# Optimization experiments

Measured on AMD Instinct MI355X. Metric: run time of the kernel, lower is better.

## Reference

```python
import jax, jax.numpy as jnp
import numpy as np

# Config: b=2, n=1024, dim=512, heads=8, dim_head=64, L=8 slices/head, temperature=0.1

def setup_inputs() -> dict:
    key = jax.random.key(0)
    ks = jax.random.split(key, 5)
    b, n, dim = 2, 1024, 512
    heads, dim_head, L = 8, 64, 8
    inner = heads * dim_head
    x = jax.random.normal(ks[0], (b, n, dim), jnp.float32)
    W_qkv = jax.random.normal(ks[1], (dim, 3 * inner), jnp.float32) * 0.02
    theta = jax.random.normal(ks[2], (heads, L, dim_head), jnp.float32)
    W_out = jax.random.normal(ks[3], (inner, dim), jnp.float32) * 0.02
    b_out = jnp.zeros((dim,), jnp.float32)
    return {"x": x, "W_qkv": W_qkv, "theta": theta, "W_out": W_out, "b_out": b_out}


def reference(x, W_qkv, theta, W_out, b_out):
    b, n, dim = x.shape
    heads, L, dim_head = theta.shape
    scale = dim_head ** -0.5
    temperature = 0.1
    # QKV projection (no bias) and head split: b n (h d) -> b h n d
    qkv = x @ W_qkv
    q, k, v = jnp.split(qkv, 3, axis=-1)
    sh = lambda t: t.reshape(b, n, heads, dim_head).transpose(0, 2, 1, 3)
    q = sh(q) * scale
    k = sh(k) * scale
    v = sh(v)
    # Esp: learnable unit slice directions per head, 1D projections
    th = theta / jnp.linalg.norm(theta, axis=-1, keepdims=True)  # [h, L, d]
    qp = jnp.einsum('bhnd,hld->bhln', q, th)  # [b,h,L,n]
    kp = jnp.einsum('bhnd,hld->bhln', k, th)
    # per-slice soft 1D transport plan (rows sum to 1), averaged over slices,
    # scaled to total-mass-1 plan (rows sum 1/n)
    d2 = (qp[..., :, None] - kp[..., None, :]) ** 2  # [b,h,L,n,n]
    plans = jax.nn.softmax(-d2 / temperature, axis=-1)
    P = plans.mean(axis=2) / n  # [b,h,n,n], rows sum to 1/n
    # SA: attn = attn * attn.shape[-1] -> row-stochastic
    attn = P * n
    out = jnp.einsum('bhnm,bhmd->bhnd', attn, v)
    out = out.transpose(0, 2, 1, 3).reshape(b, n, heads * dim_head)
    out = out @ W_out + b_out  # to_out Linear (dropout=0 in eval)
    return out, attn
```

## Files before the change

kernel.cpp:

```cpp
#include <hip/hip_runtime.h>
#include <hip/hip_bf16.h>

#define CEXP (-14.4269504088896340736f)

typedef __attribute__((ext_vector_type(8))) short bfrag8;
typedef __attribute__((ext_vector_type(4))) float fvec4;
typedef __attribute__((ext_vector_type(8))) unsigned short ushort8;
typedef __attribute__((ext_vector_type(4))) unsigned short ushort4v;

__device__ inline unsigned short f2bf(float f) {
    unsigned u = __builtin_bit_cast(unsigned, f);
    u += 0x7fffu + ((u >> 16) & 1u);
    return (unsigned short)(u >> 16);
}
__device__ inline float bf2f(unsigned short h) {
    unsigned u = ((unsigned)h) << 16;
    return __builtin_bit_cast(float, u);
}

template <int CTRL, int RMASK>
__device__ __forceinline__ float dpp_add(float v) {
    int m = __builtin_amdgcn_update_dpp(0, __builtin_bit_cast(int, v), CTRL, RMASK, 0xf, true);
    return v + __builtin_bit_cast(float, m);
}
__device__ __forceinline__ float wave_sum64(float v) {
    v = dpp_add<0xB1,  0xf>(v);
    v = dpp_add<0x4E,  0xf>(v);
    v = dpp_add<0x141, 0xf>(v);
    v = dpp_add<0x140, 0xf>(v);
    v = dpp_add<0x142, 0xa>(v);
    v = dpp_add<0x143, 0xc>(v);
    return __builtin_bit_cast(float, __builtin_amdgcn_readlane(__builtin_bit_cast(int, v), 63));
}

__global__ __launch_bounds__(256) void k_wproj(const float* __restrict__ Wqkv,
                                               const float* __restrict__ theta,
                                               const float* __restrict__ Wout,
                                               unsigned short* __restrict__ WThi,
                                               unsigned short* __restrict__ WTlo,
                                               unsigned short* __restrict__ WoThi,
                                               unsigned short* __restrict__ WoTlo) {
    __shared__ float th_s[64 * 65];
    __shared__ float ts2[64 * 65];
    __shared__ float tq[4][64];
    __shared__ float tk[4][64];
    __shared__ float wvs[4][512];
    int tid = threadIdx.x;
    int hl = tid & 63, cl = tid >> 6;
    #pragma unroll
    for (int i = 0; i < 16; ++i) {
        int r = cl * 16 + i;
        th_s[r * 65 + hl] = theta[r * 64 + hl];
    }
    __syncthreads();
    const float* ts = th_s + hl * 65;
    float ss = 0.f;
    #pragma unroll 8
    for (int d = 0; d < 64; ++d) ss = fmaf(ts[d], ts[d], ss);
    float inv = rsqrtf(ss);
    int c0b = blockIdx.x * 4;
    int c = c0b + cl;
    int h = hl >> 3;
    const float* wq = Wqkv + c * 1536 + h * 64;
    const float* wk = wq + 512;
    float aq = 0.f, ak = 0.f;
    #pragma unroll 4
    for (int d = 0; d < 64; ++d) {
        float tv = ts[d];
        aq = fmaf(wq[d], tv, aq);
        ak = fmaf(wk[d], tv, ak);
    }
    tq[cl][hl] = aq * inv;
    tk[cl][hl] = ak * inv;

    {
        const float4* src = (const float4*)(Wqkv + 1024);
        #pragma unroll
        for (int j = 0; j < 2; ++j) {
            int idx = j * 256 + tid;
            int rloc = idx >> 7, o4 = idx & 127;
            float4 v = src[(c0b + rloc) * 384 + o4];
            *(float4*)(&wvs[rloc][o4 * 4]) = v;
        }
    }
    __syncthreads();

    {
        int n = tid & 63, g = tid >> 6;
        const float (*tp)[64] = (g < 2) ? tq : tk;
        float vsrc[4];
        #pragma unroll
        for (int j = 0; j < 4; ++j) vsrc[j] = tp[j][n];
        ushort4v st;
        if ((g & 1) == 0) {
            #pragma unroll
            for (int j = 0; j < 4; ++j) st[j] = f2bf(vsrc[j]);
        } else {
            #pragma unroll
            for (int j = 0; j < 4; ++j) {
                unsigned short hi = f2bf(vsrc[j]);
                st[j] = f2bf(vsrc[j] - bf2f(hi));
            }
        }
        unsigned short* base = ((g & 1) == 0) ? WThi : WTlo;
        int nrow = (g < 2) ? n : (64 + n);
        *(ushort4v*)(base + (size_t)nrow * 512 + c0b) = st;
    }
    #pragma unroll
    for (int j2 = 0; j2 < 2; ++j2) {
        int n = j2 * 256 + tid;
        ushort4v h4, l4;
        #pragma unroll
        for (int k = 0; k < 4; ++k) {
            float v = wvs[k][n];
            unsigned short hi = f2bf(v);
            h4[k] = hi;
            l4[k] = f2bf(v - bf2f(hi));
        }
        *(ushort4v*)(WThi + (size_t)(128 + n) * 512 + c0b) = h4;
        *(ushort4v*)(WTlo + (size_t)(128 + n) * 512 + c0b) = l4;
    }

    if (blockIdx.x < 64) {
        int r0 = (blockIdx.x >> 3) * 64;
        int c0 = (blockIdx.x & 7) * 64;
        int cc = tid & 63, rr = tid >> 6;
        #pragma unroll
        for (int k = 0; k < 16; ++k) {
            int r = rr + 4 * k;
            ts2[r * 65 + cc] = Wout[(r0 + r) * 512 + c0 + cc];
        }
        __syncthreads();
        int kk = tid & 63, nn = tid >> 6;
        #pragma unroll
        for (int i = 0; i < 16; ++i) {
            int n = nn + 4 * i;
            float v = ts2[kk * 65 + n];
            unsigned short hi = f2bf(v);
            WoThi[(size_t)(c0 + n) * 512 + r0 + kk] = hi;
            WoTlo[(size_t)(c0 + n) * 512 + r0 + kk] = f2bf(v - bf2f(hi));
        }
    }
}

__global__ __launch_bounds__(256) void k_proj(const float* __restrict__ x,
                                              const unsigned short* __restrict__ WThi,
                                              const unsigned short* __restrict__ WTlo,
                                              float* __restrict__ qp,
                                              float* __restrict__ kp,
                                              unsigned short* __restrict__ vThi,
                                              unsigned short* __restrict__ vTlo) {
    __shared__ unsigned short ps[32 * 512];
    int blk = blockIdx.x;
    int cs = blk % 5;
    int rg = blk / 5;
    int tid = threadIdx.x;
    int w = tid >> 6, lane = tid & 63;

    const float4* xg = (const float4*)(x + (size_t)rg * 16 * 512);
    #pragma unroll
    for (int rep = 0; rep < 8; ++rep) {
        int idx = rep * 256 + tid;
        int row = idx >> 7, c4 = idx & 127;
        float4 v = xg[idx];
        int swz = (row & 7) << 3;
        int cbase = c4 * 4;
        ushort4v h4, l4;
        float vv[4] = {v.x, v.y, v.z, v.w};
        #pragma unroll
        for (int jj = 0; jj < 4; ++jj) {
            unsigned short hi = f2bf(vv[jj]);
            h4[jj] = hi;
            l4[jj] = f2bf(vv[jj] - bf2f(hi));
        }
        *(ushort4v*)(ps + row * 512 + (cbase ^ swz))        = h4;
        *(ushort4v*)(ps + (row + 16) * 512 + (cbase ^ swz)) = l4;
    }
    __syncthreads();

    int ar  = lane & 15;
    int asw = (ar & 7) << 3;
    int ak  = (lane >> 4) * 8;
    const unsigned short* aph = ps + ar * 512;
    const unsigned short* apl = ps + (ar + 16) * 512;
    int colb = cs * 128 + w * 32;
    size_t b0 = (size_t)(colb + ar) * 512 + ak;
    size_t b1 = b0 + 16 * 512;
    fvec4 acc0 = {0.f, 0.f, 0.f, 0.f};
    fvec4 acc1 = {0.f, 0.f, 0.f, 0.f};
    #pragma unroll 4
    for (int s = 0; s < 16; ++s) {
        int ko = s * 32 + ak;
        bfrag8 ahi = *(const bfrag8*)(aph + (ko ^ asw));
        bfrag8 alo = *(const bfrag8*)(apl + (ko ^ asw));
        bfrag8 bh0 = *(const bfrag8*)(WThi + b0 + s * 32);
        bfrag8 bl0 = *(const bfrag8*)(WTlo + b0 + s * 32);
        bfrag8 bh1 = *(const bfrag8*)(WThi + b1 + s * 32);
        bfrag8 bl1 = *(const bfrag8*)(WTlo + b1 + s * 32);
        acc0 = __builtin_amdgcn_mfma_f32_16x16x32_bf16(ahi, bh0, acc0, 0, 0, 0);
        acc0 = __builtin_amdgcn_mfma_f32_16x16x32_bf16(ahi, bl0, acc0, 0, 0, 0);
        acc0 = __builtin_amdgcn_mfma_f32_16x16x32_bf16(alo, bh0, acc0, 0, 0, 0);
        acc1 = __builtin_amdgcn_mfma_f32_16x16x32_bf16(ahi, bh1, acc1, 0, 0, 0);
        acc1 = __builtin_amdgcn_mfma_f32_16x16x32_bf16(ahi, bl1, acc1, 0, 0, 0);
        acc1 = __builtin_amdgcn_mfma_f32_16x16x32_bf16(alo, bh1, acc1, 0, 0, 0);
    }

    int rowb = rg * 16 + (lane >> 4) * 4;
    int b = rowb >> 10, n = rowb & 1023;
    fvec4 accs[2] = {acc0, acc1};
    #pragma unroll
    for (int t = 0; t < 2; ++t) {
        int col = colb + t * 16 + ar;
        fvec4 a = accs[t];
        if (col < 128) {
            int hl = col & 63;
            float* dstp = (col < 64) ? qp : kp;
            fvec4 st;
            st[0] = a[0] * 0.125f; st[1] = a[1] * 0.125f;
            st[2] = a[2] * 0.125f; st[3] = a[3] * 0.125f;
            *(fvec4*)(dstp + ((size_t)((b * 8 + (hl >> 3)) * 8 + (hl & 7))) * 1024 + n) = st;
        } else {
            int vcol = col - 128;
            int h = vcol >> 6, d = vcol & 63;
            ushort4v h4, l4;
            #pragma unroll
            for (int q = 0; q < 4; ++q) {
                unsigned short hi = f2bf(a[q]);
                h4[q] = hi;
                l4[q] = f2bf(a[q] - bf2f(hi));
            }
            size_t off = (size_t)(b * 8 + h) * 65536 + (size_t)d * 1024 + n;
            *(ushort4v*)(vThi + off) = h4;
            *(ushort4v*)(vTlo + off) = l4;
        }
    }
}

__global__ __launch_bounds__(512) void k_attn_pv(const float* __restrict__ qp,
                                                 const float* __restrict__ kp,
                                                 const unsigned short* __restrict__ vThi,
                                                 const unsigned short* __restrict__ vTlo,
                                                 float* __restrict__ attn,
                                                 unsigned short* __restrict__ ohhi,
                                                 unsigned short* __restrict__ ohlo) {
    __shared__ float s_buf[8 * 1024];
    __shared__ float sc[4 * 64 * 4];
    int bx = blockIdx.x;
    int idx = bx >> 3;
    int bh = (bx & 7) * 2 + (idx >> 7);
    int rowbase = (idx & 127) * 8;
    int tid = threadIdx.x;
    int w = tid >> 6, lane = tid & 63;

    const float4* kp4 = (const float4*)(kp + bh * 8192);
    float4* kps4 = (float4*)s_buf;
    #pragma unroll
    for (int k = 0; k < 4; ++k) kps4[k * 512 + tid] = kp4[k * 512 + tid];

    int r = rowbase + w;
    float qv[8];
    #pragma unroll
    for (int l = 0; l < 8; ++l) qv[l] = qp[bh * 8192 + l * 1024 + r];
    __syncthreads();

    const fvec4 CE4 = {CEXP, CEXP, CEXP, CEXP};
    fvec4 acc4[4];
    #pragma unroll
    for (int mm = 0; mm < 4; ++mm) acc4[mm] = (fvec4){0.f, 0.f, 0.f, 0.f};

    for (int l = 0; l < 8; ++l) {
        fvec4 kv4[4], e4[4];
        #pragma unroll
        for (int mm = 0; mm < 4; ++mm)
            kv4[mm] = *(const fvec4*)(s_buf + l * 1024 + mm * 256 + lane * 4);
        float sqs = -2.f * CEXP * qv[l];
        fvec4 sq4 = {sqs, sqs, sqs, sqs};
        fvec4 sum4 = {0.f, 0.f, 0.f, 0.f};
        #pragma unroll
        for (int mm = 0; mm < 4; ++mm) {
            fvec4 k2 = (kv4[mm] * kv4[mm]) * CE4;
            fvec4 t  = sq4 * kv4[mm] + k2;
            fvec4 e;
            e[0] = __builtin_amdgcn_exp2f(t[0]);
            e[1] = __builtin_amdgcn_exp2f(t[1]);
            e[2] = __builtin_amdgcn_exp2f(t[2]);
            e[3] = __builtin_amdgcn_exp2f(t[3]);
            e4[mm] = e;
            sum4 += e;
        }
        float s = (sum4[0] + sum4[1]) + (sum4[2] + sum4[3]);
        float inv = 0.125f * __builtin_amdgcn_rcpf(wave_sum64(s));
        fvec4 inv4 = {inv, inv, inv, inv};
        #pragma unroll
        for (int mm = 0; mm < 4; ++mm) acc4[mm] = e4[mm] * inv4 + acc4[mm];
    }

    __syncthreads();

    unsigned short* ps = (unsigned short*)s_buf;
    int swz = w << 3;
    #pragma unroll
    for (int mm = 0; mm < 4; ++mm) {
        ushort4v h4, l4;
        #pragma unroll
        for (int jj = 0; jj < 4; ++jj) {
            float v = acc4[mm][jj];
            unsigned short hi = f2bf(v);
            h4[jj] = hi;
            l4[jj] = f2bf(v - bf2f(hi));
        }
        int j0 = mm * 256 + lane * 4;
        *(ushort4v*)(ps + w * 1024 + (j0 ^ swz))       = h4;
        *(ushort4v*)(ps + (w + 8) * 1024 + (j0 ^ swz)) = l4;
    }
    __syncthreads();

    float* aR = attn + ((size_t)(bh * 1024 + r)) * 1024;
    #pragma unroll
    for (int mm = 0; mm < 4; ++mm)
        __builtin_nontemporal_store(acc4[mm], (fvec4*)(aR + mm * 256 + lane * 4));

    int n0 = (w & 3) * 16;
    int kh = w >> 2;
    int ar  = lane & 15;
    int asw = (ar & 7) << 3;
    int ak  = (lane >> 4) * 8;
    const unsigned short* ap = ps + ar * 1024;
    size_t boff = (size_t)bh * 65536 + (size_t)(n0 + ar) * 1024 + ak;
    const unsigned short* bh_p = vThi + boff;
    const unsigned short* bl_p = vTlo + boff;
    fvec4 c2 = {0.f, 0.f, 0.f, 0.f};
    #pragma unroll 4
    for (int s = kh * 16; s < kh * 16 + 16; ++s) {
        bfrag8 a  = *(const bfrag8*)(ap + ((s * 32 + ak) ^ asw));
        bfrag8 vh = *(const bfrag8*)(bh_p + s * 32);
        bfrag8 vl = *(const bfrag8*)(bl_p + s * 32);
        c2 = __builtin_amdgcn_mfma_f32_16x16x32_bf16(a, vh, c2, 0, 0, 0);
        c2 = __builtin_amdgcn_mfma_f32_16x16x32_bf16(a, vl, c2, 0, 0, 0);
    }
    if (w >= 4) {
        #pragma unroll
        for (int q = 0; q < 4; ++q) sc[(w - 4) * 256 + lane * 4 + q] = c2[q];
    }
    __syncthreads();
    if (w < 4) {
        int b = bh >> 3, h = bh & 7;
        #pragma unroll
        for (int q = 0; q < 4; ++q) {
            float t = c2[q] + sc[w * 256 + lane * 4 + q];
            t += __shfl_xor(t, 32);
            if (lane < 32) {
                int row = rowbase + (lane >> 4) * 4 + q;
                size_t o = (size_t)(b * 1024 + row) * 512 + h * 64 + n0 + ar;
                unsigned short hi = f2bf(t);
                ohhi[o] = hi;
                ohlo[o] = f2bf(t - bf2f(hi));
            }
        }
    }
}

__global__ __launch_bounds__(256) void k_out(const unsigned short* __restrict__ ohhi,
                                             const unsigned short* __restrict__ ohlo,
                                             const unsigned short* __restrict__ WoThi,
                                             const unsigned short* __restrict__ WoTlo,
                                             const float* __restrict__ bout,
                                             float* __restrict__ out) {
    __shared__ unsigned short ps[32 * 512];
    int blk = blockIdx.x;
    int cs = blk & 3;
    int rg = blk >> 2;
    int tid = threadIdx.x;
    int w = tid >> 6, lane = tid & 63;

    const ushort8* ogh = (const ushort8*)(ohhi + (size_t)rg * 16 * 512);
    const ushort8* ogl = (const ushort8*)(ohlo + (size_t)rg * 16 * 512);
    #pragma unroll
    for (int rep = 0; rep < 4; ++rep) {
        int idx = rep * 256 + tid;
        int row = idx >> 6, c8 = (idx & 63) * 8;
        int swz = (row & 7) << 3;
        *(ushort8*)(ps + row * 512 + (c8 ^ swz))        = ogh[idx];
        *(ushort8*)(ps + (row + 16) * 512 + (c8 ^ swz)) = ogl[idx];
    }
    __syncthreads();

    int ar  = lane & 15;
    int asw = (ar & 7) << 3;
    int ak  = (lane >> 4) * 8;
    const unsigned short* aph = ps + ar * 512;
    const unsigned short* apl = ps + (ar + 16) * 512;
    int colb = cs * 128 + w * 32;
    size_t b0 = (size_t)(colb + ar) * 512 + ak;
    size_t b1 = b0 + 16 * 512;
    fvec4 acc0 = {0.f, 0.f, 0.f, 0.f};
    fvec4 acc1 = {0.f, 0.f, 0.f, 0.f};
    #pragma unroll 4
    for (int s = 0; s < 16; ++s) {
        int ko = s * 32 + ak;
        bfrag8 ahi = *(const bfrag8*)(aph + (ko ^ asw));
        bfrag8 alo = *(const bfrag8*)(apl + (ko ^ asw));
        bfrag8 bh0 = *(const bfrag8*)(WoThi + b0 + s * 32);
        bfrag8 bl0 = *(const bfrag8*)(WoTlo + b0 + s * 32);
        bfrag8 bh1 = *(const bfrag8*)(WoThi + b1 + s * 32);
        bfrag8 bl1 = *(const bfrag8*)(WoTlo + b1 + s * 32);
        acc0 = __builtin_amdgcn_mfma_f32_16x16x32_bf16(ahi, bh0, acc0, 0, 0, 0);
        acc0 = __builtin_amdgcn_mfma_f32_16x16x32_bf16(ahi, bl0, acc0, 0, 0, 0);
        acc0 = __builtin_amdgcn_mfma_f32_16x16x32_bf16(alo, bh0, acc0, 0, 0, 0);
        acc1 = __builtin_amdgcn_mfma_f32_16x16x32_bf16(ahi, bh1, acc1, 0, 0, 0);
        acc1 = __builtin_amdgcn_mfma_f32_16x16x32_bf16(ahi, bl1, acc1, 0, 0, 0);
        acc1 = __builtin_amdgcn_mfma_f32_16x16x32_bf16(alo, bh1, acc1, 0, 0, 0);
    }
    int rowb = rg * 16 + (lane >> 4) * 4;
    int col0 = colb + ar;
    float bias0 = bout[col0], bias1 = bout[col0 + 16];
    #pragma unroll
    for (int q = 0; q < 4; ++q) {
        out[(rowb + q) * 512 + col0]      = acc0[q] + bias0;
        out[(rowb + q) * 512 + col0 + 16] = acc1[q] + bias1;
    }
}

extern "C" void kernel_launch(void* const* d_in, const int* in_sizes, int n_in,
                              void* d_out, int out_size, void* d_ws, size_t ws_size,
                              hipStream_t stream) {
    const float* x     = (const float*)d_in[0];
    const float* Wqkv  = (const float*)d_in[1];
    const float* theta = (const float*)d_in[2];
    const float* Wout  = (const float*)d_in[3];
    const float* bout  = (const float*)d_in[4];

    float* out  = (float*)d_out;
    float* attn = out + 2 * 1024 * 512;

    float* ws  = (float*)d_ws;
    float* qp  = ws + 65536;
    float* kp  = ws + 196608;
    unsigned short* vThi = (unsigned short*)(ws + 327680);
    unsigned short* vTlo = (unsigned short*)(ws + 851968);
    unsigned short* ohhi = (unsigned short*)(ws + 1376256);
    unsigned short* ohlo = (unsigned short*)(ws + 1900544);
    unsigned short* WoThi = (unsigned short*)(ws + 2686976);
    unsigned short* WoTlo = (unsigned short*)(ws + 2818048);
    unsigned short* WThi  = (unsigned short*)(ws + 2949120);
    unsigned short* WTlo  = (unsigned short*)(ws + 3112960);

    k_wproj   <<<128,  256, 0, stream>>>(Wqkv, theta, Wout, WThi, WTlo, WoThi, WoTlo);
    k_proj    <<<640,  256, 0, stream>>>(x, WThi, WTlo, qp, kp, vThi, vTlo);
    k_attn_pv <<<2048, 512, 0, stream>>>(qp, kp, vThi, vTlo, attn, ohhi, ohlo);
    k_out     <<<512,  256, 0, stream>>>(ohhi, ohlo, WoThi, WoTlo, bout, out);
}
```

Measured before the change: 126.7 us.

## Process two query rows per wave in fused attention-PV kernel

Each block now handles 16 query rows instead of 8: every wave computes two attention rows and reuses the same key-projection values from LDS for both, halving the grid size. The PV MFMA stage runs in two passes over 8-row tiles, with a sync between staging and compute. This amortizes the K-projection LDS load per block and the k² work across two rows. In exchange it doubles accumulator register pressure and adds extra barriers.

```diff
diff --git a/kernel.cpp b/kernel.cpp
--- a/kernel.cpp
+++ b/kernel.cpp
@@ -247,8 +247,8 @@
     __shared__ float sc[4 * 64 * 4];
     int bx = blockIdx.x;
     int idx = bx >> 3;
-    int bh = (bx & 7) * 2 + (idx >> 7);
-    int rowbase = (idx & 127) * 8;
+    int bh = (bx & 7) * 2 + (idx >> 6);
+    int rowbase = (idx & 63) * 16;
     int tid = threadIdx.x;
     int w = tid >> 6, lane = tid & 63;
 
@@ -257,106 +257,137 @@
     #pragma unroll
     for (int k = 0; k < 4; ++k) kps4[k * 512 + tid] = kp4[k * 512 + tid];
 
-    int r = rowbase + w;
-    float qv[8];
-    #pragma unroll
-    for (int l = 0; l < 8; ++l) qv[l] = qp[bh * 8192 + l * 1024 + r];
+    int rA = rowbase + 2 * w, rB = rA + 1;
+    float qvA[8], qvB[8];
+    #pragma unroll
+    for (int l = 0; l < 8; ++l) {
+        qvA[l] = qp[bh * 8192 + l * 1024 + rA];
+        qvB[l] = qp[bh * 8192 + l * 1024 + rB];
+    }
     __syncthreads();
 
     const fvec4 CE4 = {CEXP, CEXP, CEXP, CEXP};
-    fvec4 acc4[4];
-    #pragma unroll
-    for (int mm = 0; mm < 4; ++mm) acc4[mm] = (fvec4){0.f, 0.f, 0.f, 0.f};
+    fvec4 accA[4], accB[4];
+    #pragma unroll
+    for (int mm = 0; mm < 4; ++mm) {
+        accA[mm] = (fvec4){0.f, 0.f, 0.f, 0.f};
+        accB[mm] = (fvec4){0.f, 0.f, 0.f, 0.f};
+    }
 
     for (int l = 0; l < 8; ++l) {
-        fvec4 kv4[4], e4[4];
+        fvec4 kv4[4], eA[4], eB[4];
         #pragma unroll
         for (int mm = 0; mm < 4; ++mm)
             kv4[mm] = *(const fvec4*)(s_buf + l * 1024 + mm * 256 + lane * 4);
-        float sqs = -2.f * CEXP * qv[l];
-        fvec4 sq4 = {sqs, sqs, sqs, sqs};
-        fvec4 sum4 = {0.f, 0.f, 0.f, 0.f};
+        float sa = -2.f * CEXP * qvA[l];
+        float sb = -2.f * CEXP * qvB[l];
+        fvec4 sA4 = {sa, sa, sa, sa};
+        fvec4 sB4 = {sb, sb, sb, sb};
+        fvec4 sumA = {0.f, 0.f, 0.f, 0.f}, sumB = {0.f, 0.f, 0.f, 0.f};
         #pragma unroll
         for (int mm = 0; mm < 4; ++mm) {
             fvec4 k2 = (kv4[mm] * kv4[mm]) * CE4;
-            fvec4 t  = sq4 * kv4[mm] + k2;
-            fvec4 e;
-            e[0] = __builtin_amdgcn_exp2f(t[0]);
-            e[1] = __builtin_amdgcn_exp2f(t[1]);
-            e[2] = __builtin_amdgcn_exp2f(t[2]);
-            e[3] = __builtin_amdgcn_exp2f(t[3]);
-            e4[mm] = e;
-            sum4 += e;
-        }
-        float s = (sum4[0] + sum4[1]) + (sum4[2] + sum4[3]);
-        float inv = 0.125f * __builtin_amdgcn_rcpf(wave_sum64(s));
-        fvec4 inv4 = {inv, inv, inv, inv};
-        #pragma unroll
-        for (int mm = 0; mm < 4; ++mm) acc4[mm] = e4[mm] * inv4 + acc4[mm];
-    }
-
-    __syncthreads();
-
-    unsigned short* ps = (unsigned short*)s_buf;
-    int swz = w << 3;
+            fvec4 tA = sA4 * kv4[mm] + k2;
+            fvec4 tB = sB4 * kv4[mm] + k2;
+            fvec4 ea, eb;
+            ea[0] = __builtin_amdgcn_exp2f(tA[0]); eb[0] = __builtin_amdgcn_exp2f(tB[0]);
+            ea[1] = __builtin_amdgcn_exp2f(tA[1]); eb[1] = __builtin_amdgcn_exp2f(tB[1]);
+            ea[2] = __builtin_amdgcn_exp2f(tA[2]); eb[2] = __builtin_amdgcn_exp2f(tB[2]);
+            ea[3] = __builtin_amdgcn_exp2f(tA[3]); eb[3] = __builtin_amdgcn_exp2f(tB[3]);
+            eA[mm] = ea; eB[mm] = eb;
+            sumA += ea; sumB += eb;
+        }
+        float sAs = (sumA[0] + sumA[1]) + (sumA[2] + sumA[3]);
+        float sBs = (sumB[0] + sumB[1]) + (sumB[2] + sumB[3]);
+        float rAs = wave_sum64(sAs);
+        float rBs = wave_sum64(sBs);
+        float invA = 0.125f * __builtin_amdgcn_rcpf(rAs);
+        float invB = 0.125f * __builtin_amdgcn_rcpf(rBs);
+        fvec4 iA = {invA, invA, invA, invA};
+        fvec4 iB = {invB, invB, invB, invB};
+        #pragma unroll
+        for (int mm = 0; mm < 4; ++mm) {
+            accA[mm] = eA[mm] * iA + accA[mm];
+            accB[mm] = eB[mm] * iB + accB[mm];
+        }
+    }
+
+    __syncthreads();
+
+    float* aRA = attn + ((size_t)(bh * 1024 + rA)) * 1024;
+    float* aRB = attn + ((size_t)(bh * 1024 + rB)) * 1024;
     #pragma unroll
     for (int mm = 0; mm < 4; ++mm) {
-        ushort4v h4, l4;
-        #pragma unroll
-        for (int jj = 0; jj < 4; ++jj) {
-            float v = acc4[mm][jj];
-            unsigned short hi = f2bf(v);
-            h4[jj] = hi;
-            l4[jj] = f2bf(v - bf2f(hi));
-        }
-        int j0 = mm * 256 + lane * 4;
-        *(ushort4v*)(ps + w * 1024 + (j0 ^ swz))       = h4;
-        *(ushort4v*)(ps + (w + 8) * 1024 + (j0 ^ swz)) = l4;
-    }
-    __syncthreads();
-
-    float* aR = attn + ((size_t)(bh * 1024 + r)) * 1024;
-    #pragma unroll
-    for (int mm = 0; mm < 4; ++mm)
-        __builtin_nontemporal_store(acc4[mm], (fvec4*)(aR + mm * 256 + lane * 4));
-
+        __builtin_nontemporal_store(accA[mm], (fvec4*)(aRA + mm * 256 + lane * 4));
+        __builtin_nontemporal_store(accB[mm], (fvec4*)(aRB + mm * 256 + lane * 4));
+    }
+
+    unsigned short* psb = (unsigned short*)s_buf;
+    int b = bh >> 3, h = bh & 7;
     int n0 = (w & 3) * 16;
     int kh = w >> 2;
     int ar  = lane & 15;
     int asw = (ar & 7) << 3;
     int ak  = (lane >> 4) * 8;
-    const unsigned short* ap = ps + ar * 1024;
+    const unsigned short* ap = psb + ar * 1024;
     size_t boff = (size_t)bh * 65536 + (size_t)(n0 + ar) * 1024 + ak;
     const unsigned short* bh_p = vThi + boff;
     const unsigned short* bl_p = vTlo + boff;
-    fvec4 c2 = {0.f, 0.f, 0.f, 0.f};
-    #pragma unroll 4
-    for (int s = kh * 16; s < kh * 16 + 16; ++s) {
-        bfrag8 a  = *(const bfrag8*)(ap + ((s * 32 + ak) ^ asw));
-        bfrag8 vh = *(const bfrag8*)(bh_p + s * 32);
-        bfrag8 vl = *(const bfrag8*)(bl_p + s * 32);
-        c2 = __builtin_amdgcn_mfma_f32_16x16x32_bf16(a, vh, c2, 0, 0, 0);
-        c2 = __builtin_amdgcn_mfma_f32_16x16x32_bf16(a, vl, c2, 0, 0, 0);
-    }
-    if (w >= 4) {
-        #pragma unroll
-        for (int q = 0; q < 4; ++q) sc[(w - 4) * 256 + lane * 4 + q] = c2[q];
-    }
-    __syncthreads();
-    if (w < 4) {
-        int b = bh >> 3, h = bh & 7;
-        #pragma unroll
-        for (int q = 0; q < 4; ++q) {
-            float t = c2[q] + sc[w * 256 + lane * 4 + q];
-            t += __shfl_xor(t, 32);
-            if (lane < 32) {
-                int row = rowbase + (lane >> 4) * 4 + q;
-                size_t o = (size_t)(b * 1024 + row) * 512 + h * 64 + n0 + ar;
-                unsigned short hi = f2bf(t);
-                ohhi[o] = hi;
-                ohlo[o] = f2bf(t - bf2f(hi));
+
+    #pragma unroll
+    for (int pass = 0; pass < 2; ++pass) {
+        if ((w >> 2) == pass) {
+            int wl = w & 3;
+            int lr0 = 2 * wl, lr1 = lr0 + 1;
+            int swz0 = lr0 << 3, swz1 = lr1 << 3;
+            #pragma unroll
+            for (int mm = 0; mm < 4; ++mm) {
+                ushort4v hA, lA, hB, lB;
+                #pragma unroll
+                for (int jj = 0; jj < 4; ++jj) {
+                    float vA = accA[mm][jj], vB = accB[mm][jj];
+                    unsigned short hiA = f2bf(vA), hiB = f2bf(vB);
+                    hA[jj] = hiA; lA[jj] = f2bf(vA - bf2f(hiA));
+                    hB[jj] = hiB; lB[jj] = f2bf(vB - bf2f(hiB));
+                }
+                int j0 = mm * 256 + lane * 4;
+                *(ushort4v*)(psb + lr0 * 1024 + (j0 ^ swz0))       = hA;
+                *(ushort4v*)(psb + (lr0 + 8) * 1024 + (j0 ^ swz0)) = lA;
+                *(ushort4v*)(psb + lr1 * 1024 + (j0 ^ swz1))       = hB;
+                *(ushort4v*)(psb + (lr1 + 8) * 1024 + (j0 ^ swz1)) = lB;
             }
         }
+        __syncthreads();
+
+        fvec4 c2 = {0.f, 0.f, 0.f, 0.f};
+        #pragma unroll 4
+        for (int s = kh * 16; s < kh * 16 + 16; ++s) {
+            bfrag8 a  = *(const bfrag8*)(ap + ((s * 32 + ak) ^ asw));
+            bfrag8 vh = *(const bfrag8*)(bh_p + s * 32);
+            bfrag8 vl = *(const bfrag8*)(bl_p + s * 32);
+            c2 = __builtin_amdgcn_mfma_f32_16x16x32_bf16(a, vh, c2, 0, 0, 0);
+            c2 = __builtin_amdgcn_mfma_f32_16x16x32_bf16(a, vl, c2, 0, 0, 0);
+        }
+        if (w >= 4) {
+            #pragma unroll
+            for (int q = 0; q < 4; ++q) sc[(w - 4) * 256 + lane * 4 + q] = c2[q];
+        }
+        __syncthreads();
+        if (w < 4) {
+            #pragma unroll
+            for (int q = 0; q < 4; ++q) {
+                float t = c2[q] + sc[w * 256 + lane * 4 + q];
+                t += __shfl_xor(t, 32);
+                if (lane < 32) {
+                    int row = rowbase + pass * 8 + (lane >> 4) * 4 + q;
+                    size_t o = (size_t)(b * 1024 + row) * 512 + h * 64 + n0 + ar;
+                    unsigned short hi = f2bf(t);
+                    ohhi[o] = hi;
+                    ohlo[o] = f2bf(t - bf2f(hi));
+                }
+            }
+        }
+        __syncthreads();
     }
 }
 
@@ -447,6 +478,6 @@
 
     k_wproj   <<<128,  256, 0, stream>>>(Wqkv, theta, Wout, WThi, WTlo, WoThi, WoTlo);
     k_proj    <<<640,  256, 0, stream>>>(x, WThi, WTlo, qp, kp, vThi, vTlo);
-    k_attn_pv <<<2048, 512, 0, stream>>>(qp, kp, vThi, vTlo, attn, ohhi, ohlo);
+    k_attn_pv <<<1024, 512, 0, stream>>>(qp, kp, vThi, vTlo, attn, ohhi, ohlo);
     k_out     <<<512,  256, 0, stream>>>(ohhi, ohlo, WoThi, WoTlo, bout, out);
 }
```

Result: slower. 132.7 us (+4.8%).
